# Performance work log

Hardware: AMD Instinct MI355X
Metric: run time of the kernel (lower is better)

The kernel has to match this reference:

```python
import jax, jax.numpy as jnp
import numpy as np

B, SEQ, L, NK, NCLS = 4096, 8, 2048, 256, 100
LEN_VOCAB, IPD_VOCAB, EBIT, EBDIN = 1500, 256, 16, 4
C, D = 8, 4  # MM codebook groups / group dim


def setup_inputs() -> dict:
    key = jax.random.key(0)
    ks = jax.random.split(key, 16)
    f32 = jnp.float32
    return {
        'x': jax.random.randint(ks[0], (B, SEQ, 2), 0, 256, dtype=jnp.int64),
        'len_emb': jax.random.normal(ks[1], (LEN_VOCAB, EBIT), f32),
        'ipd_emb': jax.random.normal(ks[2], (IPD_VOCAB, EBIT), f32),
        'W1': jax.random.normal(ks[3], (2 * EBIT, EBDIN), f32) * 0.1,
        'b1': jax.random.normal(ks[4], (EBDIN,), f32) * 0.1,
        'We': jax.random.normal(ks[5], (EBDIN, L), f32) * 0.1,
        'be': jax.random.normal(ks[6], (L,), f32) * 0.1,
        'w3': jax.random.normal(ks[7], (NK, 3, L), f32) * 0.02,
        'w4': jax.random.normal(ks[8], (NK, 4, L), f32) * 0.02,
        'w5': jax.random.normal(ks[9], (NK, 5, L), f32) * 0.02,
        'W2': jax.random.normal(ks[10], (15 * NK, NCLS), f32) * 0.02,
        'b2': jax.random.normal(ks[11], (NCLS,), f32) * 0.02,
        'S': jax.random.normal(ks[12], (C, D, 15), f32),
        'H': jax.random.normal(ks[13], (15, 16), f32),
        'T': jax.random.normal(ks[14], (C, 15), f32),
        'LUT': jax.random.normal(ks[15], (C, 16, D), f32),
    }


def _mm(h, S, H, T, LUT):
    # h: [B, C, D]
    m = jnp.einsum('bcd,cdk->bck', h, S) - T - 0.0001
    t = jnp.tanh(m)
    m = t + jax.lax.stop_gradient(jnp.sign(m) - t)  # straight-through sign
    m = jnp.einsum('bck,kj->bcj', m, H)             # [B, C, 16]
    oh = jax.nn.one_hot(jnp.argmax(m, -1), 16, dtype=m.dtype)
    sm = jax.nn.softmax(m, -1)                      # temperature = 1
    xo = jnp.einsum('bck,ckd->bcd', oh, LUT)
    xs = jnp.einsum('bck,ckd->bcd', sm, LUT)
    return xs + jax.lax.stop_gradient(xo - xs)      # straight-through one-hot


def _segment_conv(g, ws):
    # g: [B, 8, L]. Original loops i=0..7 building an input with only row i
    # nonzero, then Conv2d(kernel=(K,L), bias=False)+ReLU and sums the 8 results.
    # With a single nonzero row, conv output at position p is x[i]@w[i-p] when
    # p <= i <= p+K-1 and 0 otherwise (relu(0)=0), so the sum over i equals a
    # diagonal gather of relu of the per-row projections -- exact same math.
    Bn = g.shape[0]
    feats = []
    for w in ws:  # w: [nk, K, L]
        K = w.shape[1]
        P = 8 - K + 1
        proj = jax.nn.relu(jnp.einsum('bhl,nkl->bhnk', g, w))  # [B,8,nk,K]
        xk = sum(proj[:, k:k + P, :, k] for k in range(K))      # [B,P,nk]
        feats.append(jnp.transpose(xk, (0, 2, 1)).reshape(Bn, -1))  # (nk,P) order
    return jnp.concatenate(feats, -1)  # [B, 15*nk]


def reference(x, len_emb, ipd_emb, W1, b1, We, be, w3, w4, w5, W2, b2, S, H, T, LUT):
    Bn = x.shape[0]
    le = len_emb[x[:, :, 0]]                        # [B, 8, 16]
    ie = ipd_emb[x[:, :, 1]]                        # [B, 8, 16]
    h = jnp.concatenate([le, ie], -1) @ W1 + b1     # [B, 8, 4]
    m = _mm(h.reshape(Bn, C, D), S, H, T, LUT)      # [B, 8, 4]
    g = m @ We + be                                 # [B, 8, L]
    f = _segment_conv(g, (w3, w4, w5))              # [B, 15*nk]
    logits = f @ W2 + b2
    return jax.nn.log_softmax(logits, -1)
```

## Files before the change

### kernel.cpp

```cpp
#include <hip/hip_runtime.h>
#include <math.h>


__global__ void k_Rz(const float* __restrict__ We, const float* __restrict__ be,
                     const float* __restrict__ w3, const float* __restrict__ w4,
                     const float* __restrict__ w5, const float* __restrict__ LUT,
                     float* __restrict__ R, float* __restrict__ G) {
  int tid = threadIdx.x;
  if (blockIdx.x == 0) {
    for (int i = tid; i < 12800; i += 256) G[i] = 0.f;
  }
  int lane = tid & 63;
  int nk = blockIdx.x * 4 + (tid >> 6);
  const float* wrow;
  if (nk < 768)       wrow = w3 + nk * 2048;
  else if (nk < 1792) wrow = w4 + (nk - 768) * 2048;
  else                wrow = w5 + (nk - 1792) * 2048;
  float a0 = 0.f, a1 = 0.f, a2 = 0.f, a3 = 0.f, a4 = 0.f;
  const float4* wp  = (const float4*)wrow;
  const float4* e0p = (const float4*)(We);
  const float4* e1p = (const float4*)(We + 2048);
  const float4* e2p = (const float4*)(We + 4096);
  const float4* e3p = (const float4*)(We + 6144);
  const float4* bep = (const float4*)(be);
#pragma unroll
  for (int i = lane; i < 512; i += 64) {
    float4 w = wp[i];
    float4 e0 = e0p[i], e1 = e1p[i], e2 = e2p[i], e3 = e3p[i], bb = bep[i];
    a0 += w.x * e0.x + w.y * e0.y + w.z * e0.z + w.w * e0.w;
    a1 += w.x * e1.x + w.y * e1.y + w.z * e1.z + w.w * e1.w;
    a2 += w.x * e2.x + w.y * e2.y + w.z * e2.z + w.w * e2.w;
    a3 += w.x * e3.x + w.y * e3.y + w.z * e3.z + w.w * e3.w;
    a4 += w.x * bb.x + w.y * bb.y + w.z * bb.z + w.w * bb.w;
  }
#pragma unroll
  for (int off = 32; off > 0; off >>= 1) {
    a0 += __shfl_xor(a0, off, 64);
    a1 += __shfl_xor(a1, off, 64);
    a2 += __shfl_xor(a2, off, 64);
    a3 += __shfl_xor(a3, off, 64);
    a4 += __shfl_xor(a4, off, 64);
  }
#pragma unroll
  for (int r = 0; r < 2; r++) {
    int rr = lane + r * 64;
    const float* lut = LUT + rr * 4;
    float v = a4 + lut[0] * a0 + lut[1] * a1 + lut[2] * a2 + lut[3] * a3;
    R[rr * 3072 + nk] = fmaxf(v, 0.f);
  }
}

__global__ void k_G(const float* __restrict__ R, const float* __restrict__ W2,
                    float* __restrict__ G) {
  int h = blockIdx.x;
  int z = blockIdx.y;
  int c = threadIdx.x;
  int nk0 = z * 64;
  int K, P, rowbase, n0, k0;
  if (nk0 < 768)       { K = 3; P = 6; rowbase = 0;    n0 = nk0 / 3;  k0 = nk0 - n0 * 3; }
  else if (nk0 < 1792) { K = 4; P = 5; rowbase = 1536; int t2 = nk0 - 768;  n0 = t2 >> 2; k0 = t2 & 3; }
  else                 { K = 5; P = 4; rowbase = 2816; int t2 = nk0 - 1792; n0 = t2 / 5;  k0 = t2 - n0 * 5; }
  float acc[16];
#pragma unroll
  for (int j = 0; j < 16; j++) acc[j] = 0.f;
  bool act = c < 100;
  const float* Rh = R + h * 16 * 3072;
  int n = n0, k = k0;
#pragma unroll
  for (int it = 0; it < 64; ++it) {
    int nk = nk0 + it;
    int p = h - k;
    if (p >= 0 && p < P) {
      float w2v = act ? W2[(rowbase + n * P + p) * 100 + c] : 0.f;
      const float* Rp = Rh + nk;
#pragma unroll
      for (int j = 0; j < 16; j++) acc[j] += Rp[j * 3072] * w2v;
    }
    if (++k == K) { k = 0; ++n; }
  }
  if (act) {
#pragma unroll
    for (int j = 0; j < 16; j++) atomicAdd(&G[(h * 16 + j) * 100 + c], acc[j]);
  }
}

__global__ void k_out(const int* __restrict__ x, const float* __restrict__ len_emb,
                      const float* __restrict__ ipd_emb, const float* __restrict__ W1,
                      const float* __restrict__ b1, const float* __restrict__ S,
                      const float* __restrict__ Hm, const float* __restrict__ T,
                      const float* __restrict__ G, const float* __restrict__ b2,
                      float* __restrict__ out) {
  int b = blockIdx.x * 4 + (threadIdx.x >> 6);
  int t = threadIdx.x & 63;
  int bj = 0;
  if (t < 8) {
    int pos = t;
    int bh = b * 8 + pos;
    bool is64 = true;
#pragma unroll
    for (int q = 0; q < 16; q++) is64 = is64 && (x[2 * q + 1] == 0);
    int i0, i1;
    if (is64) { i0 = x[4 * bh]; i1 = x[4 * bh + 2]; }
    else      { i0 = x[2 * bh]; i1 = x[2 * bh + 1]; }
    const float* le = len_emb + i0 * 16;
    const float* ie = ipd_emb + i1 * 16;
    float hv[4];
#pragma unroll
    for (int d = 0; d < 4; d++) hv[d] = b1[d];
    for (int i = 0; i < 16; i++) {
      float lv = le[i], iv = ie[i];
#pragma unroll
      for (int d = 0; d < 4; d++) hv[d] += lv * W1[i * 4 + d] + iv * W1[(16 + i) * 4 + d];
    }
    float sg[15];
#pragma unroll
    for (int kk = 0; kk < 15; kk++) {
      float m = -1e-4f - T[pos * 15 + kk];
#pragma unroll
      for (int d = 0; d < 4; d++) m += hv[d] * S[(pos * 4 + d) * 15 + kk];
      sg[kk] = (m > 0.f) ? 1.f : ((m < 0.f) ? -1.f : 0.f);
    }
    float bv = -INFINITY;
    for (int j = 0; j < 16; j++) {
      float v = 0.f;
#pragma unroll
      for (int kk = 0; kk < 15; kk++) v += sg[kk] * Hm[kk * 16 + j];
      if (v > bv) { bv = v; bj = j; }
    }
  }
  int js[8];
#pragma unroll
  for (int p = 0; p < 8; p++) js[p] = __shfl(bj, p, 64);
  int c0 = t, c1 = t + 64;
  float v0, v1 = -INFINITY;
  {
    float a = b2[c0];
#pragma unroll
    for (int p = 0; p < 8; p++) a += G[(p * 16 + js[p]) * 100 + c0];
    v0 = a;
  }
  if (c1 < 100) {
    float a = b2[c1];
#pragma unroll
    for (int p = 0; p < 8; p++) a += G[(p * 16 + js[p]) * 100 + c1];
    v1 = a;
  }
  float mx = fmaxf(v0, v1);
#pragma unroll
  for (int off = 32; off > 0; off >>= 1) mx = fmaxf(mx, __shfl_xor(mx, off, 64));
  float e = expf(v0 - mx) + ((c1 < 100) ? expf(v1 - mx) : 0.f);
#pragma unroll
  for (int off = 32; off > 0; off >>= 1) e += __shfl_xor(e, off, 64);
  float lse = mx + logf(e);
  out[b * 100 + c0] = v0 - lse;
  if (c1 < 100) out[b * 100 + c1] = v1 - lse;
}

extern "C" void kernel_launch(void* const* d_in, const int* in_sizes, int n_in,
                              void* d_out, int out_size, void* d_ws, size_t ws_size,
                              hipStream_t stream) {
  const int*   x       = (const int*)  d_in[0];
  const float* len_emb = (const float*)d_in[1];
  const float* ipd_emb = (const float*)d_in[2];
  const float* W1      = (const float*)d_in[3];
  const float* b1      = (const float*)d_in[4];
  const float* We      = (const float*)d_in[5];
  const float* be      = (const float*)d_in[6];
  const float* w3      = (const float*)d_in[7];
  const float* w4      = (const float*)d_in[8];
  const float* w5      = (const float*)d_in[9];
  const float* W2      = (const float*)d_in[10];
  const float* b2      = (const float*)d_in[11];
  const float* S       = (const float*)d_in[12];
  const float* Hm      = (const float*)d_in[13];
  const float* T       = (const float*)d_in[14];
  const float* LUT     = (const float*)d_in[15];
  float* out = (float*)d_out;

  float* R = (float*)d_out;
  float* G = (float*)d_ws;

  k_Rz<<<768, 256, 0, stream>>>(We, be, w3, w4, w5, LUT, R, G);
  dim3 gB(8, 48);
  k_G<<<gB, 128, 0, stream>>>(R, W2, G);
  k_out<<<1024, 256, 0, stream>>>(x, len_emb, ipd_emb, W1, b1, S, Hm, T, G, b2, out);
}
```

Measured before the change: 136.5 us.

## Transpose R layout, split k_G grid finer, parallelize per-position MM in k_out

```diff
diff --git a/kernel.cpp b/kernel.cpp
--- a/kernel.cpp
+++ b/kernel.cpp
@@ -46,7 +46,7 @@
     int rr = lane + r * 64;
     const float* lut = LUT + rr * 4;
     float v = a4 + lut[0] * a0 + lut[1] * a1 + lut[2] * a2 + lut[3] * a3;
-    R[rr * 3072 + nk] = fmaxf(v, 0.f);
+    R[nk * 128 + rr] = fmaxf(v, 0.f);
   }
 }
 
@@ -55,7 +55,7 @@
   int h = blockIdx.x;
   int z = blockIdx.y;
   int c = threadIdx.x;
-  int nk0 = z * 64;
+  int nk0 = z * 32;
   int K, P, rowbase, n0, k0;
   if (nk0 < 768)       { K = 3; P = 6; rowbase = 0;    n0 = nk0 / 3;  k0 = nk0 - n0 * 3; }
   else if (nk0 < 1792) { K = 4; P = 5; rowbase = 1536; int t2 = nk0 - 768;  n0 = t2 >> 2; k0 = t2 & 3; }
@@ -64,17 +64,19 @@
 #pragma unroll
   for (int j = 0; j < 16; j++) acc[j] = 0.f;
   bool act = c < 100;
-  const float* Rh = R + h * 16 * 3072;
   int n = n0, k = k0;
 #pragma unroll
-  for (int it = 0; it < 64; ++it) {
+  for (int it = 0; it < 32; ++it) {
     int nk = nk0 + it;
     int p = h - k;
     if (p >= 0 && p < P) {
       float w2v = act ? W2[(rowbase + n * P + p) * 100 + c] : 0.f;
-      const float* Rp = Rh + nk;
-#pragma unroll
-      for (int j = 0; j < 16; j++) acc[j] += Rp[j * 3072] * w2v;
+      const float4* Rp = (const float4*)(R + nk * 128 + h * 16);
+      float4 r0 = Rp[0], r1 = Rp[1], r2 = Rp[2], r3 = Rp[3];
+      acc[0]  += r0.x * w2v; acc[1]  += r0.y * w2v; acc[2]  += r0.z * w2v; acc[3]  += r0.w * w2v;
+      acc[4]  += r1.x * w2v; acc[5]  += r1.y * w2v; acc[6]  += r1.z * w2v; acc[7]  += r1.w * w2v;
+      acc[8]  += r2.x * w2v; acc[9]  += r2.y * w2v; acc[10] += r2.z * w2v; acc[11] += r2.w * w2v;
+      acc[12] += r3.x * w2v; acc[13] += r3.y * w2v; acc[14] += r3.z * w2v; acc[15] += r3.w * w2v;
     }
     if (++k == K) { k = 0; ++n; }
   }
@@ -92,45 +94,58 @@
                       float* __restrict__ out) {
   int b = blockIdx.x * 4 + (threadIdx.x >> 6);
   int t = threadIdx.x & 63;
-  int bj = 0;
-  if (t < 8) {
-    int pos = t;
-    int bh = b * 8 + pos;
-    bool is64 = true;
-#pragma unroll
-    for (int q = 0; q < 16; q++) is64 = is64 && (x[2 * q + 1] == 0);
-    int i0, i1;
-    if (is64) { i0 = x[4 * bh]; i1 = x[4 * bh + 2]; }
-    else      { i0 = x[2 * bh]; i1 = x[2 * bh + 1]; }
-    const float* le = len_emb + i0 * 16;
-    const float* ie = ipd_emb + i1 * 16;
-    float hv[4];
-#pragma unroll
-    for (int d = 0; d < 4; d++) hv[d] = b1[d];
-    for (int i = 0; i < 16; i++) {
-      float lv = le[i], iv = ie[i];
-#pragma unroll
-      for (int d = 0; d < 4; d++) hv[d] += lv * W1[i * 4 + d] + iv * W1[(16 + i) * 4 + d];
-    }
-    float sg[15];
-#pragma unroll
-    for (int kk = 0; kk < 15; kk++) {
-      float m = -1e-4f - T[pos * 15 + kk];
-#pragma unroll
-      for (int d = 0; d < 4; d++) m += hv[d] * S[(pos * 4 + d) * 15 + kk];
-      sg[kk] = (m > 0.f) ? 1.f : ((m < 0.f) ? -1.f : 0.f);
-    }
-    float bv = -INFINITY;
-    for (int j = 0; j < 16; j++) {
-      float v = 0.f;
-#pragma unroll
-      for (int kk = 0; kk < 15; kk++) v += sg[kk] * Hm[kk * 16 + j];
-      if (v > bv) { bv = v; bj = j; }
-    }
+  int pos = t >> 3;
+  int s   = t & 7;
+  int bh = b * 8 + pos;
+  bool is64 = true;
+#pragma unroll
+  for (int q = 0; q < 16; q++) is64 = is64 && (x[2 * q + 1] == 0);
+  int i0, i1;
+  if (is64) { i0 = x[4 * bh]; i1 = x[4 * bh + 2]; }
+  else      { i0 = x[2 * bh]; i1 = x[2 * bh + 1]; }
+  const float* le = len_emb + i0 * 16;
+  const float* ie = ipd_emb + i1 * 16;
+  float hv[4] = {0.f, 0.f, 0.f, 0.f};
+#pragma unroll
+  for (int u = 0; u < 2; u++) {
+    int i = s + u * 8;
+    float lv = le[i], iv = ie[i];
+#pragma unroll
+    for (int d = 0; d < 4; d++) hv[d] += lv * W1[i * 4 + d] + iv * W1[(16 + i) * 4 + d];
+  }
+#pragma unroll
+  for (int off = 1; off < 8; off <<= 1) {
+#pragma unroll
+    for (int d = 0; d < 4; d++) hv[d] += __shfl_xor(hv[d], off, 64);
+  }
+#pragma unroll
+  for (int d = 0; d < 4; d++) hv[d] += b1[d];
+  float sg[15];
+#pragma unroll
+  for (int kk = 0; kk < 15; kk++) {
+    float m = -1e-4f - T[pos * 15 + kk];
+#pragma unroll
+    for (int d = 0; d < 4; d++) m += hv[d] * S[(pos * 4 + d) * 15 + kk];
+    sg[kk] = (m > 0.f) ? 1.f : ((m < 0.f) ? -1.f : 0.f);
+  }
+  float bv = -INFINITY; int bj = 0;
+#pragma unroll
+  for (int jj = 0; jj < 2; jj++) {
+    int j = 2 * s + jj;
+    float v = 0.f;
+#pragma unroll
+    for (int kk = 0; kk < 15; kk++) v += sg[kk] * Hm[kk * 16 + j];
+    if (v > bv) { bv = v; bj = j; }
+  }
+#pragma unroll
+  for (int off = 1; off < 8; off <<= 1) {
+    float ov = __shfl_xor(bv, off, 64);
+    int   oj = __shfl_xor(bj, off, 64);
+    if (ov > bv || (ov == bv && oj < bj)) { bv = ov; bj = oj; }
   }
   int js[8];
 #pragma unroll
-  for (int p = 0; p < 8; p++) js[p] = __shfl(bj, p, 64);
+  for (int p = 0; p < 8; p++) js[p] = __shfl(bj, p * 8, 64);
   int c0 = t, c1 = t + 64;
   float v0, v1 = -INFINITY;
   {
@@ -181,7 +196,7 @@
   float* G = (float*)d_ws;
 
   k_Rz<<<768, 256, 0, stream>>>(We, be, w3, w4, w5, LUT, R, G);
-  dim3 gB(8, 48);
+  dim3 gB(8, 96);
   k_G<<<gB, 128, 0, stream>>>(R, W2, G);
   k_out<<<1024, 256, 0, stream>>>(x, len_emb, ipd_emb, W1, b1, S, Hm, T, G, b2, out);
 }
```

New measurement: 127.2 us, median of 2. 1.07x faster.
